# Performance work log

Hardware: AMD Instinct MI355X
Metric: run time of the kernel (lower is better)

Reference implementation:

```python
import jax, jax.numpy as jnp
import numpy as np

B, H, W, C, K = 8, 224, 224, 192, 7

def setup_inputs() -> dict:
    key = jax.random.key(0)
    kx, kk = jax.random.split(key)
    x = jax.random.normal(kx, (B, H, W, C), dtype=jnp.float32)
    # lecun_normal over (C, k, k): fan_in = k*k (last dim convention aside, use simple normal scaled)
    kernel = jax.random.normal(kk, (C, K, K), dtype=jnp.float32) * (1.0 / np.sqrt(K * K))
    return {"x": x, "kernel": kernel}

def reference(x, kernel):
    # Faithful FFT-based circular depthwise conv.
    Bs, Hs, Ws, Cs = x.shape
    k = kernel.shape[1]
    center = k // 2
    idx = jnp.arange(k)
    ti_1d = (idx - center) % Hs
    tj_1d = (idx - center) % Ws
    ti, tj = jnp.meshgrid(ti_1d, tj_1d, indexing='ij')
    # scatter small kernel into (C, H, W) circularly-padded kernel
    padded_kernel = jnp.zeros((Cs, Hs, Ws), dtype=kernel.dtype).at[:, ti, tj].set(kernel)
    x_f = jnp.fft.fft2(x, axes=(1, 2))                      # (B, H, W, C) complex
    kernel_f = jnp.fft.fft2(padded_kernel, axes=(1, 2))     # (C, H, W) complex
    kernel_f = kernel_f.transpose(1, 2, 0)[None, ...]       # (1, H, W, C)
    out = jnp.fft.ifft2(x_f * kernel_f, axes=(1, 2)).real
    return out
```

## Files before the change

### kernel.cpp

```cpp
#include <hip/hip_runtime.h>


#define Bn 8
#define Hn 224
#define Wn 224
#define Cn 192
#define Kn 7
#define TW 16
#define TH 4
#define C4 (Cn/4)

__global__ void transpose_weights(const float* __restrict__ k, float* __restrict__ wT) {
    int o = blockIdx.x * 256 + threadIdx.x;
    if (o < Cn * Kn * Kn) {
        int c = o % Cn;
        int r = o / Cn;
        wT[o] = k[c * (Kn * Kn) + r];
    }
}

__global__ __launch_bounds__(192, 2)
void dwconv7x7(const float4* __restrict__ x, const float4* __restrict__ wT,
               float4* __restrict__ out) {
    const int tx = threadIdx.x;
    const int ty = threadIdx.y;

    const int lin = blockIdx.x + 14 * (blockIdx.y + 56 * blockIdx.z);
    const int b   = lin & 7;
    const int q   = lin >> 3;
    const int yt  = q % 56;
    const int xt  = q / 56;

    const int w0 = xt * TW;
    const int h  = yt * TH + ty;

    float4 acc[TW];
#pragma unroll
    for (int t = 0; t < TW; ++t) acc[t] = make_float4(0.f, 0.f, 0.f, 0.f);

    for (int i = 0; i < Kn; ++i) {
        int row = h + 3 - i;
        row += (row < 0)   ? Hn : 0;
        row -= (row >= Hn) ? Hn : 0;
        const float4* __restrict__ xrow = x + (size_t)(b * Hn + row) * (Wn * C4) + tx;

        float4 wv[Kn];
#pragma unroll
        for (int j = 0; j < Kn; ++j) wv[j] = wT[(i * Kn + j) * C4 + tx];

#pragma unroll
        for (int u = 0; u < TW + 6; ++u) {
            int col = w0 + u - 3;
            col += (col < 0)   ? Wn : 0;
            col -= (col >= Wn) ? Wn : 0;
            float4 xv = xrow[col * C4];
#pragma unroll
            for (int j = 0; j < Kn; ++j) {
                int tw = u + j - 6;
                if (tw >= 0 && tw < TW) {
                    acc[tw].x += wv[j].x * xv.x;
                    acc[tw].y += wv[j].y * xv.y;
                    acc[tw].z += wv[j].z * xv.z;
                    acc[tw].w += wv[j].w * xv.w;
                }
            }
        }
    }

    float4* __restrict__ orow = out + (size_t)(b * Hn + h) * (Wn * C4) + tx;
#pragma unroll
    for (int t = 0; t < TW; ++t) orow[(w0 + t) * C4] = acc[t];
}

extern "C" void kernel_launch(void* const* d_in, const int* in_sizes, int n_in,
                              void* d_out, int out_size, void* d_ws, size_t ws_size,
                              hipStream_t stream) {
    const float* x = (const float*)d_in[0];
    const float* k = (const float*)d_in[1];
    float* wT = (float*)d_ws;

    int nW = Cn * Kn * Kn;
    transpose_weights<<<(nW + 255) / 256, 256, 0, stream>>>(k, wT);

    dim3 grid(Wn / TW, Hn / TH, Bn);
    dim3 block(C4, TH, 1);
    dwconv7x7<<<grid, block, 0, stream>>>((const float4*)x, (const float4*)wT,
                                          (float4*)d_out);
}
```

Measured before the change: 619.6 us.

## Halve width tile, stage weights in LDS, preload input row, raise occupancy

Shrinks the per-thread output tile from 16 to 8 columns and raises the launch-bounds occupancy target from 2 to 4 blocks per SIMD. Each block now copies the whole transposed weight array into shared memory, and each input row segment is loaded into registers before the FMA loop runs. Column offsets are precomputed once per thread. The intent is to cut register pressure, improve latency hiding, and take weight loads off global memory, at the cost of more halo reloads per output and a per-block LDS fill plus barrier.

```diff
diff --git a/kernel.cpp b/kernel.cpp
--- a/kernel.cpp
+++ b/kernel.cpp
@@ -6,9 +6,10 @@
 #define Wn 224
 #define Cn 192
 #define Kn 7
-#define TW 16
+#define TW 8
 #define TH 4
 #define C4 (Cn/4)
+#define NW4 (Cn*Kn*Kn/4)
 
 __global__ void transpose_weights(const float* __restrict__ k, float* __restrict__ wT) {
     int o = blockIdx.x * 256 + threadIdx.x;
@@ -19,13 +20,19 @@
     }
 }
 
-__global__ __launch_bounds__(192, 2)
+__global__ __launch_bounds__(192, 4)
 void dwconv7x7(const float4* __restrict__ x, const float4* __restrict__ wT,
                float4* __restrict__ out) {
+    __shared__ float4 wlds[NW4];
+
     const int tx = threadIdx.x;
     const int ty = threadIdx.y;
+    const int tid = ty * C4 + tx;
 
-    const int lin = blockIdx.x + 14 * (blockIdx.y + 56 * blockIdx.z);
+    for (int o = tid; o < NW4; o += 192) wlds[o] = wT[o];
+    __syncthreads();
+
+    const int lin = blockIdx.x + 28 * (blockIdx.y + 56 * blockIdx.z);
     const int b   = lin & 7;
     const int q   = lin >> 3;
     const int yt  = q % 56;
@@ -34,35 +41,42 @@
     const int w0 = xt * TW;
     const int h  = yt * TH + ty;
 
+    int coff[TW + 6];
+#pragma unroll
+    for (int u = 0; u < TW + 6; ++u) {
+        int col = w0 + u - 3;
+        col += (col < 0)   ? Wn : 0;
+        col -= (col >= Wn) ? Wn : 0;
+        coff[u] = col * C4;
+    }
+
     float4 acc[TW];
 #pragma unroll
     for (int t = 0; t < TW; ++t) acc[t] = make_float4(0.f, 0.f, 0.f, 0.f);
 
+    const float4* __restrict__ xb = x + (size_t)b * ((size_t)Hn * Wn * C4) + tx;
+
+#pragma unroll 1
     for (int i = 0; i < Kn; ++i) {
         int row = h + 3 - i;
         row += (row < 0)   ? Hn : 0;
         row -= (row >= Hn) ? Hn : 0;
-        const float4* __restrict__ xrow = x + (size_t)(b * Hn + row) * (Wn * C4) + tx;
+        const float4* __restrict__ xrow = xb + (size_t)row * (Wn * C4);
 
-        float4 wv[Kn];
+        float4 xv[TW + 6];
 #pragma unroll
-        for (int j = 0; j < Kn; ++j) wv[j] = wT[(i * Kn + j) * C4 + tx];
+        for (int u = 0; u < TW + 6; ++u) xv[u] = xrow[coff[u]];
 
 #pragma unroll
-        for (int u = 0; u < TW + 6; ++u) {
-            int col = w0 + u - 3;
-            col += (col < 0)   ? Wn : 0;
-            col -= (col >= Wn) ? Wn : 0;
-            float4 xv = xrow[col * C4];
+        for (int j = Kn - 1; j >= 0; --j) {
+            const float4 wvj = wlds[(i * Kn + j) * C4 + tx];
 #pragma unroll
-            for (int j = 0; j < Kn; ++j) {
-                int tw = u + j - 6;
-                if (tw >= 0 && tw < TW) {
-                    acc[tw].x += wv[j].x * xv.x;
-                    acc[tw].y += wv[j].y * xv.y;
-                    acc[tw].z += wv[j].z * xv.z;
-                    acc[tw].w += wv[j].w * xv.w;
-                }
+            for (int tw = 0; tw < TW; ++tw) {
+                const float4 xvv = xv[tw + 6 - j];
+                acc[tw].x += wvj.x * xvv.x;
+                acc[tw].y += wvj.y * xvv.y;
+                acc[tw].z += wvj.z * xvv.z;
+                acc[tw].w += wvj.w * xvv.w;
             }
         }
     }
```

Measured after the change: 605.9 us. 1.02x faster.
